# Optimization experiments

Hardware: AMD Instinct MI355X
Metric: run time of the kernel (lower is better)

The kernel has to match this reference:

```python
import jax, jax.numpy as jnp
import numpy as np

B, S, D, H = 2, 2048, 768, 12
DK = D // H


def setup_inputs() -> dict:
    key = jax.random.key(0)
    ks = jax.random.split(key, 12)
    inp = {
        "q": jax.random.normal(ks[0], (B, S, D), jnp.float32),
        "k": jax.random.normal(ks[1], (B, S, D), jnp.float32),
        "v": jax.random.normal(ks[2], (B, S, D), jnp.float32),
        # float mask: 1.0 where attention is disallowed (causal upper triangle)
        "mask": (1.0 - jnp.tril(jnp.ones((S, S), jnp.float32)))[None, None],
        "Wq": jax.random.normal(ks[3], (D, D), jnp.float32) / np.sqrt(D),
        "bq": jnp.zeros((D,), jnp.float32),
        "Wk": jax.random.normal(ks[4], (D, D), jnp.float32) / np.sqrt(D),
        "bk": jnp.zeros((D,), jnp.float32),
        "Wv": jax.random.normal(ks[5], (D, D), jnp.float32) / np.sqrt(D),
        "bv": jnp.zeros((D,), jnp.float32),
        "Wo": jax.random.normal(ks[6], (D, D), jnp.float32) / np.sqrt(D),
        "bo": jnp.zeros((D,), jnp.float32),
    }
    return inp


def _split_heads(x):
    # [B,S,D] -> [B,H,S,DK]
    b, s, _ = x.shape
    return x.reshape(b, s, H, DK).transpose(0, 2, 1, 3)


def reference(q, k, v, mask, Wq, bq, Wk, bk, Wv, bv, Wo, bo):
    Q = _split_heads(q @ Wq + bq)
    K = _split_heads(k @ Wk + bk)
    V = _split_heads(v @ Wv + bv)
    scale = jax.lax.rsqrt(jnp.float32(D))  # note: d_model, not d_k (faithful)
    logits = jnp.einsum("bhqd,bhkd->bhqk", Q, K) * scale
    logits = logits + (-1e9) * mask
    weights = jax.nn.softmax(logits, axis=-1)
    attn = jnp.einsum("bhqk,bhkd->bhqd", weights, V)
    attn = attn.transpose(0, 2, 1, 3).reshape(q.shape)  # [B,S,D]
    return jax.nn.relu(attn @ Wo + bo)
```

## Files before the change

kernel.cpp:

```cpp
#include <hip/hip_runtime.h>
#include <math.h>

#define BB 2
#define SS 2048
#define DD 768
#define HH 12
#define DKK 64
#define MM (BB*SS)

typedef _Float16 half_t;
using half8 = __attribute__((ext_vector_type(8))) _Float16;
using half4 = __attribute__((ext_vector_type(4))) _Float16;
using floatx4 = __attribute__((ext_vector_type(4))) float;

__device__ __forceinline__ void gload_lds16(const half_t* g, half_t* l)
{
    auto gp = (const __attribute__((address_space(1))) half_t*)(uintptr_t)g;
    auto lp = (__attribute__((address_space(3))) half_t*)(uint32_t)(uintptr_t)l;
    __builtin_amdgcn_global_load_lds(gp, lp, 16, 0, 0);
}

__global__ __launch_bounds__(256)
void convert_qkv(const float* __restrict__ q, const float* __restrict__ k,
                 const float* __restrict__ v, half_t* __restrict__ qh,
                 half_t* __restrict__ kh, half_t* __restrict__ vh)
{
    const float* src = blockIdx.y == 0 ? q : (blockIdx.y == 1 ? k : v);
    half_t* dst      = blockIdx.y == 0 ? qh : (blockIdx.y == 1 ? kh : vh);
    int i = blockIdx.x * 256 + threadIdx.x;
    float4 f = ((const float4*)src)[i];
    half4 hv;
    hv[0] = (half_t)f.x; hv[1] = (half_t)f.y; hv[2] = (half_t)f.z; hv[3] = (half_t)f.w;
    ((half4*)dst)[i] = hv;
}

__global__ __launch_bounds__(256)
void wtrans(const float* __restrict__ W0, const float* __restrict__ W1,
            const float* __restrict__ W2, const float* __restrict__ W3,
            half_t* __restrict__ T0, half_t* __restrict__ T1,
            half_t* __restrict__ T2, half_t* __restrict__ T3)
{
    int z = blockIdx.z;
    const float* W = z == 0 ? W0 : z == 1 ? W1 : z == 2 ? W2 : W3;
    half_t* T      = z == 0 ? T0 : z == 1 ? T1 : z == 2 ? T2 : T3;

    __shared__ float tile[64][68];
    int k0 = blockIdx.x * 64, n0 = blockIdx.y * 64;
    int t = threadIdx.x;
    #pragma unroll
    for (int i = 0; i < 4; ++i) {
        int c = t + i * 256;
        int kr = c >> 4, nc = (c & 15) * 4;
        *(float4*)&tile[kr][nc] = *(const float4*)&W[(size_t)(k0 + kr) * DD + n0 + nc];
    }
    __syncthreads();
    #pragma unroll
    for (int i = 0; i < 4; ++i) {
        int c = t + i * 256;
        int nr = c >> 4, kc = (c & 15) * 4;
        half4 hv;
        #pragma unroll
        for (int j = 0; j < 4; ++j) hv[j] = (half_t)tile[kc + j][nr];
        *(half4*)&T[(size_t)(n0 + nr) * DD + k0 + kc] = hv;
    }
}

template<bool SWAP>
__device__ __forceinline__
void gemm_body(const half_t* __restrict__ A, const half_t* __restrict__ Bt,
               floatx4 (&acc)[4][4], half_t (*As)[32], half_t (*Bs)[32],
               int m0, int n0)
{
    const int t = threadIdx.x;
    const int lane = t & 63, wave = t >> 6;
    const int lr = lane & 15, lq = lane >> 4;
    const int wm = (wave >> 1) * 64, wn = (wave & 1) * 64;
    const int srow0 = wave * 32 + (lane >> 2);
    const int scol  = (lane & 3) * 8;

    #pragma unroll
    for (int mi = 0; mi < 4; ++mi)
        #pragma unroll
        for (int ni = 0; ni < 4; ++ni)
            #pragma unroll
            for (int r = 0; r < 4; ++r) acc[mi][ni][r] = 0.f;

    for (int k0 = 0; k0 < DD; k0 += 32) {
        __syncthreads();
        #pragma unroll
        for (int j = 0; j < 2; ++j) {
            int row = srow0 + j * 16;
            gload_lds16(&A [(size_t)(m0 + row) * DD + k0 + scol], &As[row][scol]);
            gload_lds16(&Bt[(size_t)(n0 + row) * DD + k0 + scol], &Bs[row][scol]);
        }
        __builtin_amdgcn_s_waitcnt(0x0f70);
        __syncthreads();

        half8 af[4], bf[4];
        #pragma unroll
        for (int i = 0; i < 4; ++i) {
            af[i] = *(const half8*)&As[wm + i * 16 + lr][lq * 8];
            bf[i] = *(const half8*)&Bs[wn + i * 16 + lr][lq * 8];
        }
        #pragma unroll
        for (int mi = 0; mi < 4; ++mi)
            #pragma unroll
            for (int ni = 0; ni < 4; ++ni) {
                if (SWAP)
                    acc[mi][ni] = __builtin_amdgcn_mfma_f32_16x16x32_f16(
                        bf[ni], af[mi], acc[mi][ni], 0, 0, 0);
                else
                    acc[mi][ni] = __builtin_amdgcn_mfma_f32_16x16x32_f16(
                        af[mi], bf[ni], acc[mi][ni], 0, 0, 0);
            }
    }
}

__global__ __launch_bounds__(256)
void proj_gemm(const half_t* __restrict__ qh, const half_t* __restrict__ kh,
               const half_t* __restrict__ vh,
               const half_t* __restrict__ Wqt, const half_t* __restrict__ Wkt,
               const half_t* __restrict__ Wvt,
               const float* __restrict__ bq, const float* __restrict__ bk,
               const float* __restrict__ bv,
               half_t* __restrict__ Qo, half_t* __restrict__ Ko,
               half_t* __restrict__ Vto)
{
    const int z = blockIdx.z;
    const half_t* A  = z == 0 ? qh  : z == 1 ? kh  : vh;
    const half_t* Bt = z == 0 ? Wqt : z == 1 ? Wkt : Wvt;
    const float* bias = z == 0 ? bq : z == 1 ? bk : bv;

    __shared__ half_t As[128][32];
    __shared__ half_t Bs[128][32];
    floatx4 acc[4][4];
    const int m0 = blockIdx.y * 128, n0 = blockIdx.x * 128;

    if (z == 2) gemm_body<true >(A, Bt, acc, As, Bs, m0, n0);
    else        gemm_body<false>(A, Bt, acc, As, Bs, m0, n0);

    const int lane = threadIdx.x & 63, wave = threadIdx.x >> 6;
    const int lr = lane & 15, lq = lane >> 4;
    const int wm = (wave >> 1) * 64, wn = (wave & 1) * 64;

    if (z == 2) {
        #pragma unroll
        for (int mi = 0; mi < 4; ++mi)
            #pragma unroll
            for (int ni = 0; ni < 4; ++ni)
                #pragma unroll
                for (int r = 0; r < 4; ++r) {
                    int dcol = n0 + wn + ni * 16 + lq * 4 + r;
                    int srow = m0 + wm + mi * 16 + lr;
                    int hh = dcol >> 6, d = dcol & 63;
                    int b2 = srow >> 11, sdx = srow & 2047;
                    Vto[((size_t)((b2 * HH + hh) * DKK + d)) * SS + sdx] =
                        (half_t)(acc[mi][ni][r] + bias[dcol]);
                }
    } else {
        const float sc = (z == 0) ? 0.03608439182435161f : 1.0f;
        half_t* O = z == 0 ? Qo : Ko;
        #pragma unroll
        for (int mi = 0; mi < 4; ++mi)
            #pragma unroll
            for (int ni = 0; ni < 4; ++ni)
                #pragma unroll
                for (int r = 0; r < 4; ++r) {
                    int row = m0 + wm + mi * 16 + lq * 4 + r;
                    int col = n0 + wn + ni * 16 + lr;
                    O[(size_t)row * DD + col] = (half_t)((acc[mi][ni][r] + bias[col]) * sc);
                }
    }
}

__global__ __launch_bounds__(256)
void out_gemm(const half_t* __restrict__ A, const half_t* __restrict__ Bt,
              const float* __restrict__ bias, float* __restrict__ C)
{
    __shared__ half_t As[128][32];
    __shared__ half_t Bs[128][32];
    floatx4 acc[4][4];
    const int m0 = blockIdx.y * 128, n0 = blockIdx.x * 128;
    gemm_body<false>(A, Bt, acc, As, Bs, m0, n0);

    const int lane = threadIdx.x & 63, wave = threadIdx.x >> 6;
    const int lr = lane & 15, lq = lane >> 4;
    const int wm = (wave >> 1) * 64, wn = (wave & 1) * 64;

    #pragma unroll
    for (int mi = 0; mi < 4; ++mi)
        #pragma unroll
        for (int ni = 0; ni < 4; ++ni)
            #pragma unroll
            for (int r = 0; r < 4; ++r) {
                int row = m0 + wm + mi * 16 + lq * 4 + r;
                int col = n0 + wn + ni * 16 + lr;
                C[(size_t)row * DD + col] = fmaxf(acc[mi][ni][r] + bias[col], 0.f);
            }
}

__global__ __launch_bounds__(128)
void attn_split(const half_t* __restrict__ Qf, const half_t* __restrict__ Kf,
                const half_t* __restrict__ Vt, half_t* __restrict__ Of,
                float* __restrict__ Opart, float* __restrict__ Lpart)
{
    __shared__ half_t Ks[64][72];
    __shared__ half_t Vs[64][72];
    __shared__ half_t Ps[2][32][72];

    const int i = blockIdx.x;
    const int bh = i % 24;
    const int j = i / 24;
    int qt, c; bool single;
    if (j < 16) { qt = 15 - j; c = 0; single = true; }
    else        { int jj = j - 16; qt = 31 - (jj >> 1); c = jj & 1; single = false; }
    const int kt0 = c * 16;
    const int kt1 = (!single && c == 0) ? 16 : (qt + 1);

    const int b = bh / HH, h = bh % HH;
    const int t = threadIdx.x;
    const int lane = t & 63, wave = t >> 6;
    const int lr = lane & 15, lq = lane >> 4;
    const int q0 = qt * 64;

    half8 qa[2][2];
    #pragma unroll
    for (int qg = 0; qg < 2; ++qg) {
        const half_t* qptr =
            Qf + ((size_t)(b * SS + q0 + wave * 32 + qg * 16 + lr)) * DD + h * DKK;
        qa[qg][0] = *(const half8*)(qptr + lq * 8);
        qa[qg][1] = *(const half8*)(qptr + 32 + lq * 8);
    }

    floatx4 o[2][4];
    #pragma unroll
    for (int qg = 0; qg < 2; ++qg)
        #pragma unroll
        for (int nt = 0; nt < 4; ++nt)
            #pragma unroll
            for (int r = 0; r < 4; ++r) o[qg][nt][r] = 0.f;
    float l_run[2] = {0.f, 0.f};

    for (int kt = kt0; kt < kt1; ++kt) {
        __syncthreads();
        #pragma unroll
        for (int ii = 0; ii < 4; ++ii) {
            int cc = t + ii * 128;
            int row = cc >> 3, c8 = (cc & 7) * 8;
            *(half8*)&Ks[row][c8] =
                *(const half8*)&Kf[((size_t)(b * SS + kt * 64 + row)) * DD + h * DKK + c8];
            *(half8*)&Vs[row][c8] =
                *(const half8*)&Vt[((size_t)((b * HH + h) * DKK + row)) * SS + kt * 64 + c8];
        }
        __syncthreads();

        floatx4 s[2][4];
        #pragma unroll
        for (int nt = 0; nt < 4; ++nt) {
            half8 kf0 = *(const half8*)&Ks[nt * 16 + lr][lq * 8];
            half8 kf1 = *(const half8*)&Ks[nt * 16 + lr][32 + lq * 8];
            #pragma unroll
            for (int qg = 0; qg < 2; ++qg) {
                floatx4 a = {0.f, 0.f, 0.f, 0.f};
                a = __builtin_amdgcn_mfma_f32_16x16x32_f16(kf0, qa[qg][0], a, 0, 0, 0);
                a = __builtin_amdgcn_mfma_f32_16x16x32_f16(kf1, qa[qg][1], a, 0, 0, 0);
                s[qg][nt] = a;
            }
        }

        if (kt == qt) {
            #pragma unroll
            for (int qg = 0; qg < 2; ++qg) {
                int qrow = q0 + wave * 32 + qg * 16 + lr;
                #pragma unroll
                for (int nt = 0; nt < 4; ++nt)
                    #pragma unroll
                    for (int r = 0; r < 4; ++r) {
                        int key = kt * 64 + nt * 16 + lq * 4 + r;
                        if (key > qrow) s[qg][nt][r] = -1e30f;
                    }
            }
        }

        #pragma unroll
        for (int qg = 0; qg < 2; ++qg)
            #pragma unroll
            for (int nt = 0; nt < 4; ++nt) {
                half4 hp;
                #pragma unroll
                for (int r = 0; r < 4; ++r) {
                    float p = __expf(s[qg][nt][r]);
                    l_run[qg] += p;
                    hp[r] = (half_t)p;
                }
                *(half4*)&Ps[wave][qg * 16 + lr][nt * 16 + lq * 4] = hp;
            }

        __builtin_amdgcn_s_waitcnt(0xc07f);

        half8 pa[2][2];
        #pragma unroll
        for (int qg = 0; qg < 2; ++qg) {
            pa[qg][0] = *(const half8*)&Ps[wave][qg * 16 + lr][lq * 8];
            pa[qg][1] = *(const half8*)&Ps[wave][qg * 16 + lr][32 + lq * 8];
        }

        #pragma unroll
        for (int nt = 0; nt < 4; ++nt) {
            half8 vf0 = *(const half8*)&Vs[nt * 16 + lr][lq * 8];
            half8 vf1 = *(const half8*)&Vs[nt * 16 + lr][32 + lq * 8];
            #pragma unroll
            for (int qg = 0; qg < 2; ++qg) {
                o[qg][nt] = __builtin_amdgcn_mfma_f32_16x16x32_f16(vf0, pa[qg][0], o[qg][nt], 0, 0, 0);
                o[qg][nt] = __builtin_amdgcn_mfma_f32_16x16x32_f16(vf1, pa[qg][1], o[qg][nt], 0, 0, 0);
            }
        }
    }

    #pragma unroll
    for (int qg = 0; qg < 2; ++qg) {
        l_run[qg] += __shfl_xor(l_run[qg], 16);
        l_run[qg] += __shfl_xor(l_run[qg], 32);
    }

    if (single) {
        #pragma unroll
        for (int qg = 0; qg < 2; ++qg) {
            float inv = 1.f / l_run[qg];
            int qrow = q0 + wave * 32 + qg * 16 + lr;
            #pragma unroll
            for (int nt = 0; nt < 4; ++nt) {
                half4 hv;
                #pragma unroll
                for (int r = 0; r < 4; ++r) hv[r] = (half_t)(o[qg][nt][r] * inv);
                *(half4*)&Of[((size_t)(b * SS + qrow)) * DD + h * DKK + nt * 16 + lq * 4] = hv;
            }
        }
    } else {
        const int p = (bh * 16 + (qt - 16)) * 2 + c;
        float* Ob = Opart + (size_t)p * 4096;
        #pragma unroll
        for (int qg = 0; qg < 2; ++qg) {
            int qq = wave * 32 + qg * 16 + lr;
            #pragma unroll
            for (int nt = 0; nt < 4; ++nt)
                *(floatx4*)&Ob[qq * 64 + nt * 16 + lq * 4] = o[qg][nt];
            if (lq == 0) Lpart[p * 64 + qq] = l_run[qg];
        }
    }
}

__global__ __launch_bounds__(256)
void attn_combine(const float* __restrict__ Opart, const float* __restrict__ Lpart,
                  half_t* __restrict__ Of)
{
    const int ib = blockIdx.x;
    const int bh = ib >> 4, qtm = ib & 15;
    const int b = bh / HH, h = bh % HH;
    const int p0 = (bh * 16 + qtm) * 2, p1 = p0 + 1;
    const int t = threadIdx.x;
    const int q = t >> 2, ds0 = (t & 3) * 16;

    float inv = 1.f / (Lpart[p0 * 64 + q] + Lpart[p1 * 64 + q]);
    const float* O0 = Opart + (size_t)p0 * 4096 + q * 64 + ds0;
    const float* O1 = Opart + (size_t)p1 * 4096 + q * 64 + ds0;
    int srow = (qtm + 16) * 64 + q;
    half_t* dst = Of + ((size_t)(b * SS + srow)) * DD + h * DKK + ds0;

    #pragma unroll
    for (int kk = 0; kk < 4; ++kk) {
        float4 a = *(const float4*)&O0[kk * 4];
        float4 c = *(const float4*)&O1[kk * 4];
        half4 hv;
        hv[0] = (half_t)((a.x + c.x) * inv);
        hv[1] = (half_t)((a.y + c.y) * inv);
        hv[2] = (half_t)((a.z + c.z) * inv);
        hv[3] = (half_t)((a.w + c.w) * inv);
        *(half4*)&dst[kk * 4] = hv;
    }
}

extern "C" void kernel_launch(void* const* d_in, const int* in_sizes, int n_in,
                              void* d_out, int out_size, void* d_ws, size_t ws_size,
                              hipStream_t stream)
{
    (void)in_sizes; (void)n_in; (void)out_size; (void)ws_size;
    const float* q  = (const float*)d_in[0];
    const float* k  = (const float*)d_in[1];
    const float* v  = (const float*)d_in[2];
    const float* Wq = (const float*)d_in[4];
    const float* bq = (const float*)d_in[5];
    const float* Wk = (const float*)d_in[6];
    const float* bk = (const float*)d_in[7];
    const float* Wv = (const float*)d_in[8];
    const float* bv = (const float*)d_in[9];
    const float* Wo = (const float*)d_in[10];
    const float* bo = (const float*)d_in[11];
    float* out = (float*)d_out;

    half_t* qh  = (half_t*)d_ws;
    half_t* kh  = qh  + (size_t)MM * DD;
    half_t* vh  = kh  + (size_t)MM * DD;
    half_t* Wqt = vh  + (size_t)MM * DD;
    half_t* Wkt = Wqt + (size_t)DD * DD;
    half_t* Wvt = Wkt + (size_t)DD * DD;
    half_t* Wot = Wvt + (size_t)DD * DD;
    half_t* Qo  = Wot + (size_t)DD * DD;
    half_t* Ko  = Qo  + (size_t)MM * DD;
    half_t* Vto = Ko  + (size_t)MM * DD;
    half_t* Ao  = Vto + (size_t)MM * DD;

    float* Opart = (float*)d_ws;
    float* Lpart = Opart + (size_t)768 * 4096;

    convert_qkv<<<dim3(MM * DD / 4 / 256, 3), 256, 0, stream>>>(q, k, v, qh, kh, vh);
    wtrans<<<dim3(DD / 64, DD / 64, 4), 256, 0, stream>>>(Wq, Wk, Wv, Wo, Wqt, Wkt, Wvt, Wot);
    proj_gemm<<<dim3(DD / 128, MM / 128, 3), 256, 0, stream>>>(
        qh, kh, vh, Wqt, Wkt, Wvt, bq, bk, bv, Qo, Ko, Vto);
    attn_split<<<dim3(24 * 48), 128, 0, stream>>>(Qo, Ko, Vto, Ao, Opart, Lpart);
    attn_combine<<<dim3(384), 256, 0, stream>>>(Opart, Lpart, Ao);
    out_gemm<<<dim3(DD / 128, MM / 128), 256, 0, stream>>>(Ao, Wot, bo, out);
}
```

Before: 242.5 us.

## Merge prep kernels, retile GEMMs to 128x64xK64, enlarge attention query tiles with prefetch

The input conversion and weight transpose kernels are merged into one launch. The GEMMs switch to 128x64 output tiles with a K step of 64, padded LDS rows and plain vector loads in place of direct global-to-LDS loads. Attention now uses 128-query tiles with 256 threads, register prefetch of the next K/V tile, and a rebalanced causal split with matching combine indexing. This trades fewer launches, more parallel GEMM blocks and overlapped loads against losing the async LDS load path and a reworked work split.

```diff
diff --git a/kernel.cpp b/kernel.cpp
--- a/kernel.cpp
+++ b/kernel.cpp
@@ -13,106 +13,111 @@
 using half4 = __attribute__((ext_vector_type(4))) _Float16;
 using floatx4 = __attribute__((ext_vector_type(4))) float;
 
-__device__ __forceinline__ void gload_lds16(const half_t* g, half_t* l)
-{
-    auto gp = (const __attribute__((address_space(1))) half_t*)(uintptr_t)g;
-    auto lp = (__attribute__((address_space(3))) half_t*)(uint32_t)(uintptr_t)l;
-    __builtin_amdgcn_global_load_lds(gp, lp, 16, 0, 0);
-}
-
 __global__ __launch_bounds__(256)
-void convert_qkv(const float* __restrict__ q, const float* __restrict__ k,
-                 const float* __restrict__ v, half_t* __restrict__ qh,
-                 half_t* __restrict__ kh, half_t* __restrict__ vh)
-{
-    const float* src = blockIdx.y == 0 ? q : (blockIdx.y == 1 ? k : v);
-    half_t* dst      = blockIdx.y == 0 ? qh : (blockIdx.y == 1 ? kh : vh);
-    int i = blockIdx.x * 256 + threadIdx.x;
-    float4 f = ((const float4*)src)[i];
-    half4 hv;
-    hv[0] = (half_t)f.x; hv[1] = (half_t)f.y; hv[2] = (half_t)f.z; hv[3] = (half_t)f.w;
-    ((half4*)dst)[i] = hv;
-}
-
-__global__ __launch_bounds__(256)
-void wtrans(const float* __restrict__ W0, const float* __restrict__ W1,
-            const float* __restrict__ W2, const float* __restrict__ W3,
-            half_t* __restrict__ T0, half_t* __restrict__ T1,
-            half_t* __restrict__ T2, half_t* __restrict__ T3)
-{
-    int z = blockIdx.z;
-    const float* W = z == 0 ? W0 : z == 1 ? W1 : z == 2 ? W2 : W3;
-    half_t* T      = z == 0 ? T0 : z == 1 ? T1 : z == 2 ? T2 : T3;
-
+void prep(const float* __restrict__ q, const float* __restrict__ k,
+          const float* __restrict__ v,
+          const float* __restrict__ Wq, const float* __restrict__ Wk,
+          const float* __restrict__ Wv, const float* __restrict__ Wo,
+          half_t* __restrict__ qh, half_t* __restrict__ kh,
+          half_t* __restrict__ vh,
+          half_t* __restrict__ Wqt, half_t* __restrict__ Wkt,
+          half_t* __restrict__ Wvt, half_t* __restrict__ Wot)
+{
     __shared__ float tile[64][68];
-    int k0 = blockIdx.x * 64, n0 = blockIdx.y * 64;
-    int t = threadIdx.x;
-    #pragma unroll
-    for (int i = 0; i < 4; ++i) {
-        int c = t + i * 256;
-        int kr = c >> 4, nc = (c & 15) * 4;
-        *(float4*)&tile[kr][nc] = *(const float4*)&W[(size_t)(k0 + kr) * DD + n0 + nc];
-    }
-    __syncthreads();
-    #pragma unroll
-    for (int i = 0; i < 4; ++i) {
-        int c = t + i * 256;
-        int nr = c >> 4, kc = (c & 15) * 4;
+    const int y = blockIdx.y;
+    const int t = threadIdx.x;
+    if (y < 3) {
+        const float* src = y == 0 ? q : (y == 1 ? k : v);
+        half_t* dst      = y == 0 ? qh : (y == 1 ? kh : vh);
+        int i = blockIdx.x * 256 + t;
+        float4 f = ((const float4*)src)[i];
         half4 hv;
-        #pragma unroll
-        for (int j = 0; j < 4; ++j) hv[j] = (half_t)tile[kc + j][nr];
-        *(half4*)&T[(size_t)(n0 + nr) * DD + k0 + kc] = hv;
+        hv[0] = (half_t)f.x; hv[1] = (half_t)f.y;
+        hv[2] = (half_t)f.z; hv[3] = (half_t)f.w;
+        ((half4*)dst)[i] = hv;
+    } else {
+        int x = blockIdx.x;
+        if (x >= 576) return;
+        int w = x / 144, rem = x % 144;
+        const float* W = w == 0 ? Wq : w == 1 ? Wk : w == 2 ? Wv : Wo;
+        half_t* T      = w == 0 ? Wqt : w == 1 ? Wkt : w == 2 ? Wvt : Wot;
+        int k0 = (rem % 12) * 64, n0 = (rem / 12) * 64;
+        #pragma unroll
+        for (int i = 0; i < 4; ++i) {
+            int c = t + i * 256;
+            int kr = c >> 4, nc = (c & 15) * 4;
+            *(float4*)&tile[kr][nc] = *(const float4*)&W[(size_t)(k0 + kr) * DD + n0 + nc];
+        }
+        __syncthreads();
+        #pragma unroll
+        for (int i = 0; i < 4; ++i) {
+            int c = t + i * 256;
+            int nr = c >> 4, kc = (c & 15) * 4;
+            half4 hv;
+            #pragma unroll
+            for (int jj = 0; jj < 4; ++jj) hv[jj] = (half_t)tile[kc + jj][nr];
+            *(half4*)&T[(size_t)(n0 + nr) * DD + k0 + kc] = hv;
+        }
     }
 }
 
 template<bool SWAP>
 __device__ __forceinline__
 void gemm_body(const half_t* __restrict__ A, const half_t* __restrict__ Bt,
-               floatx4 (&acc)[4][4], half_t (*As)[32], half_t (*Bs)[32],
+               floatx4 (&acc)[4][2], half_t (*As)[72], half_t (*Bs)[72],
                int m0, int n0)
 {
     const int t = threadIdx.x;
     const int lane = t & 63, wave = t >> 6;
     const int lr = lane & 15, lq = lane >> 4;
-    const int wm = (wave >> 1) * 64, wn = (wave & 1) * 64;
-    const int srow0 = wave * 32 + (lane >> 2);
-    const int scol  = (lane & 3) * 8;
+    const int wm = (wave >> 1) * 64, wn = (wave & 1) * 32;
+    const int a_r = t >> 1,  a_c = (t & 1) * 32;
+    const int b_r = t >> 2,  b_c = (t & 3) * 16;
 
     #pragma unroll
     for (int mi = 0; mi < 4; ++mi)
         #pragma unroll
-        for (int ni = 0; ni < 4; ++ni)
+        for (int ni = 0; ni < 2; ++ni)
             #pragma unroll
             for (int r = 0; r < 4; ++r) acc[mi][ni][r] = 0.f;
 
-    for (int k0 = 0; k0 < DD; k0 += 32) {
+    for (int k0 = 0; k0 < DD; k0 += 64) {
         __syncthreads();
         #pragma unroll
-        for (int j = 0; j < 2; ++j) {
-            int row = srow0 + j * 16;
-            gload_lds16(&A [(size_t)(m0 + row) * DD + k0 + scol], &As[row][scol]);
-            gload_lds16(&Bt[(size_t)(n0 + row) * DD + k0 + scol], &Bs[row][scol]);
-        }
-        __builtin_amdgcn_s_waitcnt(0x0f70);
+        for (int jj = 0; jj < 4; ++jj)
+            *(half8*)&As[a_r][a_c + jj * 8] =
+                *(const half8*)&A[(size_t)(m0 + a_r) * DD + k0 + a_c + jj * 8];
+        #pragma unroll
+        for (int jj = 0; jj < 2; ++jj)
+            *(half8*)&Bs[b_r][b_c + jj * 8] =
+                *(const half8*)&Bt[(size_t)(n0 + b_r) * DD + k0 + b_c + jj * 8];
         __syncthreads();
 
-        half8 af[4], bf[4];
-        #pragma unroll
-        for (int i = 0; i < 4; ++i) {
-            af[i] = *(const half8*)&As[wm + i * 16 + lr][lq * 8];
-            bf[i] = *(const half8*)&Bs[wn + i * 16 + lr][lq * 8];
-        }
+        half8 af[4][2], bf[2][2];
         #pragma unroll
         for (int mi = 0; mi < 4; ++mi)
             #pragma unroll
-            for (int ni = 0; ni < 4; ++ni) {
-                if (SWAP)
-                    acc[mi][ni] = __builtin_amdgcn_mfma_f32_16x16x32_f16(
-                        bf[ni], af[mi], acc[mi][ni], 0, 0, 0);
-                else
-                    acc[mi][ni] = __builtin_amdgcn_mfma_f32_16x16x32_f16(
-                        af[mi], bf[ni], acc[mi][ni], 0, 0, 0);
-            }
+            for (int kp = 0; kp < 2; ++kp)
+                af[mi][kp] = *(const half8*)&As[wm + mi * 16 + lr][kp * 32 + lq * 8];
+        #pragma unroll
+        for (int ni = 0; ni < 2; ++ni)
+            #pragma unroll
+            for (int kp = 0; kp < 2; ++kp)
+                bf[ni][kp] = *(const half8*)&Bs[wn + ni * 16 + lr][kp * 32 + lq * 8];
+
+        #pragma unroll
+        for (int mi = 0; mi < 4; ++mi)
+            #pragma unroll
+            for (int ni = 0; ni < 2; ++ni)
+                #pragma unroll
+                for (int kp = 0; kp < 2; ++kp) {
+                    if (SWAP)
+                        acc[mi][ni] = __builtin_amdgcn_mfma_f32_16x16x32_f16(
+                            bf[ni][kp], af[mi][kp], acc[mi][ni], 0, 0, 0);
+                    else
+                        acc[mi][ni] = __builtin_amdgcn_mfma_f32_16x16x32_f16(
+                            af[mi][kp], bf[ni][kp], acc[mi][ni], 0, 0, 0);
+                }
     }
 }
 
@@ -131,23 +136,23 @@
     const half_t* Bt = z == 0 ? Wqt : z == 1 ? Wkt : Wvt;
     const float* bias = z == 0 ? bq : z == 1 ? bk : bv;
 
-    __shared__ half_t As[128][32];
-    __shared__ half_t Bs[128][32];
-    floatx4 acc[4][4];
-    const int m0 = blockIdx.y * 128, n0 = blockIdx.x * 128;
+    __shared__ half_t As[128][72];
+    __shared__ half_t Bs[64][72];
+    floatx4 acc[4][2];
+    const int m0 = blockIdx.y * 128, n0 = blockIdx.x * 64;
 
     if (z == 2) gemm_body<true >(A, Bt, acc, As, Bs, m0, n0);
     else        gemm_body<false>(A, Bt, acc, As, Bs, m0, n0);
 
     const int lane = threadIdx.x & 63, wave = threadIdx.x >> 6;
     const int lr = lane & 15, lq = lane >> 4;
-    const int wm = (wave >> 1) * 64, wn = (wave & 1) * 64;
+    const int wm = (wave >> 1) * 64, wn = (wave & 1) * 32;
 
     if (z == 2) {
         #pragma unroll
         for (int mi = 0; mi < 4; ++mi)
             #pragma unroll
-            for (int ni = 0; ni < 4; ++ni)
+            for (int ni = 0; ni < 2; ++ni)
                 #pragma unroll
                 for (int r = 0; r < 4; ++r) {
                     int dcol = n0 + wn + ni * 16 + lq * 4 + r;
@@ -163,7 +168,7 @@
         #pragma unroll
         for (int mi = 0; mi < 4; ++mi)
             #pragma unroll
-            for (int ni = 0; ni < 4; ++ni)
+            for (int ni = 0; ni < 2; ++ni)
                 #pragma unroll
                 for (int r = 0; r < 4; ++r) {
                     int row = m0 + wm + mi * 16 + lq * 4 + r;
@@ -177,20 +182,20 @@
 void out_gemm(const half_t* __restrict__ A, const half_t* __restrict__ Bt,
               const float* __restrict__ bias, float* __restrict__ C)
 {
-    __shared__ half_t As[128][32];
-    __shared__ half_t Bs[128][32];
-    floatx4 acc[4][4];
-    const int m0 = blockIdx.y * 128, n0 = blockIdx.x * 128;
+    __shared__ half_t As[128][72];
+    __shared__ half_t Bs[64][72];
+    floatx4 acc[4][2];
+    const int m0 = blockIdx.y * 128, n0 = blockIdx.x * 64;
     gemm_body<false>(A, Bt, acc, As, Bs, m0, n0);
 
     const int lane = threadIdx.x & 63, wave = threadIdx.x >> 6;
     const int lr = lane & 15, lq = lane >> 4;
-    const int wm = (wave >> 1) * 64, wn = (wave & 1) * 64;
+    const int wm = (wave >> 1) * 64, wn = (wave & 1) * 32;
 
     #pragma unroll
     for (int mi = 0; mi < 4; ++mi)
         #pragma unroll
-        for (int ni = 0; ni < 4; ++ni)
+        for (int ni = 0; ni < 2; ++ni)
             #pragma unroll
             for (int r = 0; r < 4; ++r) {
                 int row = m0 + wm + mi * 16 + lq * 4 + r;
@@ -199,35 +204,50 @@
             }
 }
 
-__global__ __launch_bounds__(128)
+__global__ __launch_bounds__(256)
 void attn_split(const half_t* __restrict__ Qf, const half_t* __restrict__ Kf,
                 const half_t* __restrict__ Vt, half_t* __restrict__ Of,
                 float* __restrict__ Opart, float* __restrict__ Lpart)
 {
     __shared__ half_t Ks[64][72];
     __shared__ half_t Vs[64][72];
-    __shared__ half_t Ps[2][32][72];
+    __shared__ half_t Ps[4][32][72];
 
     const int i = blockIdx.x;
     const int bh = i % 24;
     const int j = i / 24;
     int qt, c; bool single;
-    if (j < 16) { qt = 15 - j; c = 0; single = true; }
-    else        { int jj = j - 16; qt = 31 - (jj >> 1); c = jj & 1; single = false; }
+    if (j < 8)       { qt = 15 - j;        c = 0; single = false; }
+    else if (j < 16) { qt = 15 - (j - 8);  c = 1; single = false; }
+    else             { qt = 7 - (j - 16);  c = 0; single = true;  }
     const int kt0 = c * 16;
-    const int kt1 = (!single && c == 0) ? 16 : (qt + 1);
+    const int kt1 = (!single && c == 0) ? 16 : (2 * qt + 2);
 
     const int b = bh / HH, h = bh % HH;
     const int t = threadIdx.x;
     const int lane = t & 63, wave = t >> 6;
     const int lr = lane & 15, lq = lane >> 4;
-    const int q0 = qt * 64;
+    const int q0 = qt * 128;
+
+    const int srow = t >> 3;
+    const int scol = (t & 7) * 8;
+
+    const half_t* Kbase = Kf + (size_t)(b * SS) * DD + h * DKK;
+    const half_t* Vbase = Vt + (size_t)((b * HH + h) * DKK) * SS;
+
+    half8 kpre[2], vpre[2];
+    #pragma unroll
+    for (int ii = 0; ii < 2; ++ii) {
+        int row = srow + ii * 32;
+        kpre[ii] = *(const half8*)&Kbase[(size_t)(kt0 * 64 + row) * DD + scol];
+        vpre[ii] = *(const half8*)&Vbase[(size_t)row * SS + kt0 * 64 + scol];
+    }
 
     half8 qa[2][2];
     #pragma unroll
     for (int qg = 0; qg < 2; ++qg) {
         const half_t* qptr =
-            Qf + ((size_t)(b * SS + q0 + wave * 32 + qg * 16 + lr)) * DD + h * DKK;
+            Qf + (size_t)(b * SS + q0 + wave * 32 + qg * 16 + lr) * DD + h * DKK;
         qa[qg][0] = *(const half8*)(qptr + lq * 8);
         qa[qg][1] = *(const half8*)(qptr + 32 + lq * 8);
     }
@@ -244,15 +264,21 @@
     for (int kt = kt0; kt < kt1; ++kt) {
         __syncthreads();
         #pragma unroll
-        for (int ii = 0; ii < 4; ++ii) {
-            int cc = t + ii * 128;
-            int row = cc >> 3, c8 = (cc & 7) * 8;
-            *(half8*)&Ks[row][c8] =
-                *(const half8*)&Kf[((size_t)(b * SS + kt * 64 + row)) * DD + h * DKK + c8];
-            *(half8*)&Vs[row][c8] =
-                *(const half8*)&Vt[((size_t)((b * HH + h) * DKK + row)) * SS + kt * 64 + c8];
+        for (int ii = 0; ii < 2; ++ii) {
+            int row = srow + ii * 32;
+            *(half8*)&Ks[row][scol] = kpre[ii];
+            *(half8*)&Vs[row][scol] = vpre[ii];
         }
         __syncthreads();
+
+        if (kt + 1 < kt1) {
+            #pragma unroll
+            for (int ii = 0; ii < 2; ++ii) {
+                int row = srow + ii * 32;
+                kpre[ii] = *(const half8*)&Kbase[(size_t)((kt + 1) * 64 + row) * DD + scol];
+                vpre[ii] = *(const half8*)&Vbase[(size_t)row * SS + (kt + 1) * 64 + scol];
+            }
+        }
 
         floatx4 s[2][4];
         #pragma unroll
@@ -268,7 +294,7 @@
             }
         }
 
-        if (kt == qt) {
+        if (kt >= 2 * qt) {
             #pragma unroll
             for (int qg = 0; qg < 2; ++qg) {
                 int qrow = q0 + wave * 32 + qg * 16 + lr;
@@ -333,19 +359,19 @@
                 half4 hv;
                 #pragma unroll
                 for (int r = 0; r < 4; ++r) hv[r] = (half_t)(o[qg][nt][r] * inv);
-                *(half4*)&Of[((size_t)(b * SS + qrow)) * DD + h * DKK + nt * 16 + lq * 4] = hv;
+                *(half4*)&Of[(size_t)(b * SS + qrow) * DD + h * DKK + nt * 16 + lq * 4] = hv;
             }
         }
     } else {
-        const int p = (bh * 16 + (qt - 16)) * 2 + c;
-        float* Ob = Opart + (size_t)p * 4096;
+        const int p = (bh * 8 + (qt - 8)) * 2 + c;
+        float* Ob = Opart + (size_t)p * 8192;
         #pragma unroll
         for (int qg = 0; qg < 2; ++qg) {
             int qq = wave * 32 + qg * 16 + lr;
             #pragma unroll
             for (int nt = 0; nt < 4; ++nt)
                 *(floatx4*)&Ob[qq * 64 + nt * 16 + lq * 4] = o[qg][nt];
-            if (lq == 0) Lpart[p * 64 + qq] = l_run[qg];
+            if (lq == 0) Lpart[p * 128 + qq] = l_run[qg];
         }
     }
 }
@@ -355,20 +381,20 @@
                   half_t* __restrict__ Of)
 {
     const int ib = blockIdx.x;
-    const int bh = ib >> 4, qtm = ib & 15;
+    const int bh = ib >> 3, qtm = ib & 7;
     const int b = bh / HH, h = bh % HH;
-    const int p0 = (bh * 16 + qtm) * 2, p1 = p0 + 1;
+    const int p0 = (bh * 8 + qtm) * 2, p1 = p0 + 1;
     const int t = threadIdx.x;
-    const int q = t >> 2, ds0 = (t & 3) * 16;
-
-    float inv = 1.f / (Lpart[p0 * 64 + q] + Lpart[p1 * 64 + q]);
-    const float* O0 = Opart + (size_t)p0 * 4096 + q * 64 + ds0;
-    const float* O1 = Opart + (size_t)p1 * 4096 + q * 64 + ds0;
-    int srow = (qtm + 16) * 64 + q;
-    half_t* dst = Of + ((size_t)(b * SS + srow)) * DD + h * DKK + ds0;
-
-    #pragma unroll
-    for (int kk = 0; kk < 4; ++kk) {
+    const int qq = t >> 1, ds0 = (t & 1) * 32;
+
+    float inv = 1.f / (Lpart[p0 * 128 + qq] + Lpart[p1 * 128 + qq]);
+    const float* O0 = Opart + (size_t)p0 * 8192 + qq * 64 + ds0;
+    const float* O1 = Opart + (size_t)p1 * 8192 + qq * 64 + ds0;
+    int srow = (qtm + 8) * 128 + qq;
+    half_t* dst = Of + (size_t)(b * SS + srow) * DD + h * DKK + ds0;
+
+    #pragma unroll
+    for (int kk = 0; kk < 8; ++kk) {
         float4 a = *(const float4*)&O0[kk * 4];
         float4 c = *(const float4*)&O1[kk * 4];
         half4 hv;
@@ -411,13 +437,13 @@
     half_t* Ao  = Vto + (size_t)MM * DD;
 
     float* Opart = (float*)d_ws;
-    float* Lpart = Opart + (size_t)768 * 4096;
-
-    convert_qkv<<<dim3(MM * DD / 4 / 256, 3), 256, 0, stream>>>(q, k, v, qh, kh, vh);
-    wtrans<<<dim3(DD / 64, DD / 64, 4), 256, 0, stream>>>(Wq, Wk, Wv, Wo, Wqt, Wkt, Wvt, Wot);
-    proj_gemm<<<dim3(DD / 128, MM / 128, 3), 256, 0, stream>>>(
+    float* Lpart = Opart + (size_t)384 * 8192;
+
+    prep<<<dim3(3072, 4), 256, 0, stream>>>(q, k, v, Wq, Wk, Wv, Wo,
+                                            qh, kh, vh, Wqt, Wkt, Wvt, Wot);
+    proj_gemm<<<dim3(DD / 64, MM / 128, 3), 256, 0, stream>>>(
         qh, kh, vh, Wqt, Wkt, Wvt, bq, bk, bv, Qo, Ko, Vto);
-    attn_split<<<dim3(24 * 48), 128, 0, stream>>>(Qo, Ko, Vto, Ao, Opart, Lpart);
-    attn_combine<<<dim3(384), 256, 0, stream>>>(Opart, Lpart, Ao);
-    out_gemm<<<dim3(DD / 128, MM / 128), 256, 0, stream>>>(Ao, Wot, bo, out);
-}
+    attn_split<<<dim3(24 * 24), 256, 0, stream>>>(Qo, Ko, Vto, Ao, Opart, Lpart);
+    attn_combine<<<dim3(192), 256, 0, stream>>>(Opart, Lpart, Ao);
+    out_gemm<<<dim3(DD / 64, MM / 128), 256, 0, stream>>>(Ao, Wot, bo, out);
+}
```

New measurement: 205.8 us. 1.18x faster.
